# Kernel tuning notes

Hardware: AMD Instinct MI355X
Metric: run time of the kernel (lower is better)

## Reference

```python
import jax, jax.numpy as jnp
import numpy as np

N_NODES = 100000
BN_EPS = 1e-5


def _linear_params(key, fan_in, fan_out):
    k1, k2 = jax.random.split(key)
    lim = 1.0 / np.sqrt(fan_in)
    W = jax.random.uniform(k1, (fan_in, fan_out), jnp.float32, -lim, lim)
    b = jax.random.uniform(k2, (fan_out,), jnp.float32, -lim, lim)
    return W, b


def setup_inputs() -> dict:
    key = jax.random.key(0)
    ks = jax.random.split(key, 24)
    in_ch, hid, tdim, L = 17, 64, 32, 2
    E = 1600000
    inp = {}
    inp["x"] = jax.random.normal(ks[0], (N_NODES, in_ch), jnp.float32)
    inp["edge_index"] = jax.random.randint(ks[1], (2, E), 0, N_NODES, jnp.int64)
    inp["edge_dts"] = jax.random.uniform(ks[2], (E,), jnp.float32) * 100.0
    inp["batch_size"] = 10000
    # TimeEncode params (learned, TGAT init)
    inp["basis_freq"] = jnp.asarray(1.0 / 10 ** np.linspace(0, 9, tdim), jnp.float32)
    inp["phase"] = jnp.zeros((tdim,), jnp.float32)
    # TMP edge MLP: in = 2*in_ch + tdim
    mi = 2 * in_ch + tdim
    inp["tmp_W1"], inp["tmp_b1"] = _linear_params(ks[3], mi, mi // 2)
    inp["tmp_W2"], inp["tmp_b2"] = _linear_params(ks[4], mi // 2, in_ch)
    inp["proj_W"], inp["proj_b"] = _linear_params(ks[5], in_ch, hid)
    # SMP layers (stacked over L)
    si = 2 * hid
    W1s, b1s, W2s, b2s = [], [], [], []
    for l in range(L):
        W1, b1 = _linear_params(ks[6 + 2 * l], si, si // 2)
        W2, b2 = _linear_params(ks[7 + 2 * l], si // 2, hid)
        W1s.append(W1); b1s.append(b1); W2s.append(W2); b2s.append(b2)
    inp["smp_W1"] = jnp.stack(W1s); inp["smp_b1"] = jnp.stack(b1s)
    inp["smp_W2"] = jnp.stack(W2s); inp["smp_b2"] = jnp.stack(b2s)
    inp["bn_gamma"] = jnp.ones((L, hid), jnp.float32)
    inp["bn_beta"] = jnp.zeros((L, hid), jnp.float32)
    # classifier head
    inp["clf_W1"], inp["clf_b1"] = _linear_params(ks[12], hid, hid)
    inp["clf_g1"] = jnp.ones((hid,), jnp.float32); inp["clf_bb1"] = jnp.zeros((hid,), jnp.float32)
    inp["clf_W2"], inp["clf_b2"] = _linear_params(ks[13], hid, hid // 2)
    inp["clf_g2"] = jnp.ones((hid // 2,), jnp.float32); inp["clf_bb2"] = jnp.zeros((hid // 2,), jnp.float32)
    inp["clf_W3"], inp["clf_b3"] = _linear_params(ks[14], hid // 2, 1)
    return inp


def _segment_mean(vals, idx, n):
    s = jax.ops.segment_sum(vals, idx, num_segments=n)
    c = jax.ops.segment_sum(jnp.ones((idx.shape[0], 1), vals.dtype), idx, num_segments=n)
    return s / jnp.maximum(c, 1.0)


def _bn(x, g, b):
    m = x.mean(0)
    v = x.var(0)
    return (x - m) * jax.lax.rsqrt(v + BN_EPS) * g + b


def reference(x, edge_index, edge_dts, batch_size, basis_freq, phase,
              tmp_W1, tmp_b1, tmp_W2, tmp_b2, proj_W, proj_b,
              smp_W1, smp_b1, smp_W2, smp_b2, bn_gamma, bn_beta,
              clf_W1, clf_b1, clf_g1, clf_bb1,
              clf_W2, clf_b2, clf_g2, clf_bb2, clf_W3, clf_b3):
    src, dst = edge_index[0], edge_index[1]  # x_j = x[src], x_i = x[dst]
    n = x.shape[0]
    # TimeEncode: cos(t * freq + phase)  -> [E, time_dim]
    rel = jnp.cos(edge_dts[:, None] * basis_freq + phase)
    # --- TMP conv (applied once) ---
    x_i = x[dst]
    m_in = jnp.concatenate([x_i, x[src], rel], axis=-1)
    p = jnp.tanh(jax.nn.relu(m_in @ tmp_W1 + tmp_b1) @ tmp_W2 + tmp_b2)
    msg = (2.0 * p - 1.0) * x_i  # (p - q) * x_i with q = 1 - p
    h = x + _segment_mean(msg, dst, n)
    # --- project to hidden ---
    h = h @ proj_W + proj_b
    # --- L SMP layers with BatchNorm + ReLU (dropout = eval/identity) ---
    L = smp_W1.shape[0]
    for l in range(L):
        h_i = h[dst]
        m_in = jnp.concatenate([h_i, h[src]], axis=-1)
        p = jnp.tanh(jax.nn.relu(m_in @ smp_W1[l] + smp_b1[l]) @ smp_W2[l] + smp_b2[l])
        h = h + _segment_mean((2.0 * p - 1.0) * h_i, dst, n)
        h = jax.nn.relu(_bn(h, bn_gamma[l], bn_beta[l]))
    # --- classifier on seed nodes ---
    z = h[:batch_size]
    z = jax.nn.relu(_bn(z @ clf_W1 + clf_b1, clf_g1, clf_bb1))
    z = jax.nn.relu(_bn(z @ clf_W2 + clf_b2, clf_g2, clf_bb2))
    return z @ clf_W3 + clf_b3  # [batch_size, 1] logits
```

## Files before the change

### kernel.cpp

```cpp
#include <hip/hip_runtime.h>
#include <hip/hip_bf16.h>


typedef float  f32x4 __attribute__((ext_vector_type(4)));
typedef short  s16x8 __attribute__((ext_vector_type(8)));

__device__ __forceinline__ float tanh_factor(float u) {
  float e = __expf(2.0f * u);
  return fmaf(-4.0f, __builtin_amdgcn_rcpf(e + 1.0f), 1.0f);
}

__device__ __forceinline__ void atomic_add_f32(float* p, float v) {
  unsafeAtomicAdd(p, v);
}

__device__ __forceinline__ unsigned short f2bf(float f) {
  __hip_bfloat16 b = __float2bfloat16(f);
  return *(unsigned short*)&b;
}
__device__ __forceinline__ float bf2f(unsigned short u) {
  unsigned int v = ((unsigned int)u) << 16;
  return *(float*)&v;
}

__global__ __launch_bounds__(256) void k_hist(
    const int* __restrict__ ei, int* __restrict__ cntI, int E)
{
  int e = blockIdx.x * 256 + threadIdx.x;
  if (e < E) atomicAdd(&cntI[ei[E + e]], 1);
}

__global__ __launch_bounds__(256) void k_scan_block(
    const int* __restrict__ cntI, int* __restrict__ cursor,
    int* __restrict__ bsum, int N)
{
  __shared__ int s[256];
  const int t = threadIdx.x;
  int i = blockIdx.x * 256 + t;
  int v = (i < N) ? cntI[i] : 0;
  s[t] = v;
  for (int off = 1; off < 256; off <<= 1) {
    __syncthreads();
    int x = (t >= off) ? s[t - off] : 0;
    __syncthreads();
    s[t] += x;
  }
  __syncthreads();
  if (i < N) cursor[i] = s[t] - v;
  if (t == 255) bsum[blockIdx.x] = s[255];
}

__global__ __launch_bounds__(512) void k_scan_bsum(int* __restrict__ bsum, int nb)
{
  __shared__ int s[512];
  const int t = threadIdx.x;
  int v = (t < nb) ? bsum[t] : 0;
  s[t] = v;
  for (int off = 1; off < 512; off <<= 1) {
    __syncthreads();
    int x = (t >= off) ? s[t - off] : 0;
    __syncthreads();
    s[t] += x;
  }
  __syncthreads();
  if (t < nb) bsum[t] = s[t] - v;
}

__global__ __launch_bounds__(256) void k_expand_add(
    int* __restrict__ cursor, const int* __restrict__ bsum,
    const int* __restrict__ cntI, int* __restrict__ dstS, int N)
{
  int n = blockIdx.x * 256 + threadIdx.x;
  if (n >= N) return;
  int cur = cursor[n] + bsum[blockIdx.x];
  cursor[n] = cur;
  int c = cntI[n];
  for (int i = 0; i < c; i++) dstS[cur + i] = n;
}

__global__ __launch_bounds__(256) void k_scatter(
    const int* __restrict__ ei, const float* __restrict__ dts,
    int* __restrict__ cursor, int2* __restrict__ srcdtS, int E)
{
  int e = blockIdx.x * 256 + threadIdx.x;
  if (e >= E) return;
  int d = ei[E + e];
  int pos = atomicAdd(&cursor[d], 1);
  srcdtS[pos] = make_int2(ei[e], __float_as_int(dts[e]));
}

__global__ __launch_bounds__(256) void prep_all(
    const float* __restrict__ x, const float* __restrict__ tW1,
    const float* __restrict__ tW2, const float* __restrict__ sW1,
    const float* __restrict__ sW2, unsigned short* __restrict__ xb,
    unsigned short* __restrict__ W1t1, unsigned short* __restrict__ W2t1,
    unsigned short* __restrict__ W1t, unsigned short* __restrict__ W2t, int N)
{
  int i = blockIdx.x * 256 + threadIdx.x;
  int totalX = N * 24;
  for (int idx = i; idx < totalX; idx += gridDim.x * 256) {
    int n = idx / 24, c = idx - n * 24;
    xb[idx] = (c < 17) ? f2bf(x[n * 17 + c]) : (unsigned short)0;
  }
  if (i < 48 * 96) {
    int n = i / 96, k = i - n * 96;
    int src = (k < 17) ? k : (k >= 24 && k < 41) ? (k - 24 + 17)
            : (k >= 48 && k < 80) ? (k - 48 + 34) : -1;
    W1t1[i] = (n < 33 && src >= 0) ? f2bf(tW1[src * 33 + n]) : (unsigned short)0;
  }
  if (i < 32 * 64) {
    int n = i / 64, k = i - n * 64;
    W2t1[i] = (n < 17 && k < 33) ? f2bf(tW2[k * 17 + n]) : (unsigned short)0;
  }
  if (i < 2 * 64 * 128) {
    int l = i >> 13; int r = i & 8191; int n = r >> 7; int k = r & 127;
    W1t[i] = f2bf(sW1[((size_t)l * 128 + k) * 64 + n]);
  }
  if (i < 2 * 64 * 64) {
    int l = i >> 12; int r = i & 4095; int n = r >> 6; int k = r & 63;
    W2t[i] = f2bf(sW2[((size_t)l * 64 + k) * 64 + n]);
  }
}

__global__ __launch_bounds__(256, 3) void phase1_edge_mfma(
    const unsigned short* __restrict__ xb, const int* __restrict__ dstS,
    const int2* __restrict__ srcdtS, const float* __restrict__ freq,
    const float* __restrict__ phs,
    const unsigned short* __restrict__ W1t1, const float* __restrict__ b1,
    const unsigned short* __restrict__ W2t1, const float* __restrict__ b2,
    float* __restrict__ accum, int E, int nwt)
{
  __shared__ unsigned short sA[64][104];
  __shared__ unsigned short sHid[64][72];
  __shared__ float sRed[64][20];
  __shared__ int   sDst[64];

  const int t = threadIdx.x;
  const int wv = t >> 6, lane = t & 63, l16 = lane & 15, quad = lane >> 4;
  const int r0 = wv * 16;

  s16x8 w1f[3][3], w2f[2][2];
  float bias1[3], bias2[2];
#pragma unroll
  for (int cb = 0; cb < 3; cb++) {
    int n = cb * 16 + l16;
#pragma unroll
    for (int kb = 0; kb < 3; kb++)
      w1f[cb][kb] = *(const s16x8*)&W1t1[n * 96 + kb * 32 + quad * 8];
    bias1[cb] = (n < 33) ? b1[n] : 0.0f;
  }
#pragma unroll
  for (int cb = 0; cb < 2; cb++) {
    int n = cb * 16 + l16;
#pragma unroll
    for (int kb = 0; kb < 2; kb++)
      w2f[cb][kb] = *(const s16x8*)&W2t1[n * 64 + kb * 32 + quad * 8];
    bias2[cb] = (n < 17) ? b2[n] : 0.0f;
  }

  for (int i = lane; i < 16 * 28; i += 64) {
    int rr = r0 + i / 28, c = i % 28;
    int col = (c < 6) ? 18 + c : (c < 12) ? 42 + (c - 6) : 80 + (c - 12);
    sA[rr][col] = 0;
  }
  for (int i = lane; i < 256; i += 64)
    sHid[r0 + (i >> 4)][48 + (i & 15)] = 0;

  const int gw = blockIdx.x * 4 + wv;
  const int nw = gridDim.x * 4;

  for (int tile = gw; tile < nwt; tile += nw) {
    const int eb = tile << 4;

    {
      int e_loc = lane >> 2, q = lane & 3;
      int rr = r0 + e_loc;
      int er = eb + e_loc; if (er >= E) er = E - 1;
      if (q < 2) {
        int node = q ? srcdtS[er].x : dstS[er];
        if (!q) sDst[rr] = node;
        const unsigned short* src = &xb[(size_t)node * 24];
        int base = q ? 24 : 0;
        *(uint4*)&sA[rr][base]     = *(const uint4*)&src[0];
        *(uint4*)&sA[rr][base + 8] = *(const uint4*)&src[8];
        *(unsigned int*)&sA[rr][base + 16] = *(const unsigned int*)&src[16];
      } else {
        float dt = __int_as_float(srcdtS[er].y);
        int k0 = (q == 2) ? 0 : 16;
        unsigned short tmp[16] __attribute__((aligned(16)));
#pragma unroll
        for (int j = 0; j < 16; j++)
          tmp[j] = f2bf(__cosf(fmaf(dt, freq[k0 + j], phs[k0 + j])));
        *(uint4*)&sA[rr][48 + k0]     = *(const uint4*)&tmp[0];
        *(uint4*)&sA[rr][48 + k0 + 8] = *(const uint4*)&tmp[8];
      }
    }

    f32x4 a1[3];
#pragma unroll
    for (int cb = 0; cb < 3; cb++)
      a1[cb] = (f32x4){bias1[cb], bias1[cb], bias1[cb], bias1[cb]};
#pragma unroll
    for (int kb = 0; kb < 3; kb++) {
      s16x8 aF = *(const s16x8*)&sA[r0 + l16][kb * 32 + quad * 8];
#pragma unroll
      for (int cb = 0; cb < 3; cb++)
        a1[cb] = __builtin_amdgcn_mfma_f32_16x16x32_bf16(aF, w1f[cb][kb], a1[cb], 0, 0, 0);
    }
#pragma unroll
    for (int cb = 0; cb < 3; cb++)
#pragma unroll
      for (int reg = 0; reg < 4; reg++)
        sHid[r0 + quad * 4 + reg][cb * 16 + l16] = f2bf(fmaxf(a1[cb][reg], 0.0f));

    f32x4 a2[2];
#pragma unroll
    for (int cb = 0; cb < 2; cb++)
      a2[cb] = (f32x4){bias2[cb], bias2[cb], bias2[cb], bias2[cb]};
#pragma unroll
    for (int kb = 0; kb < 2; kb++) {
      s16x8 aF = *(const s16x8*)&sHid[r0 + l16][kb * 32 + quad * 8];
#pragma unroll
      for (int cb = 0; cb < 2; cb++)
        a2[cb] = __builtin_amdgcn_mfma_f32_16x16x32_bf16(aF, w2f[cb][kb], a2[cb], 0, 0, 0);
    }

#pragma unroll
    for (int reg = 0; reg < 4; reg++) {
      int row = r0 + quad * 4 + reg;
      bool ok = (eb + quad * 4 + reg < E);
      sRed[row][l16] = ok ? tanh_factor(a2[0][reg]) : 0.0f;
      if (l16 == 0) sRed[row][16] = ok ? tanh_factor(a2[1][reg]) : 0.0f;
    }

    if (lane < 17) {
      int col = lane;
      float run = 0.0f;
      int cur = sDst[r0];
#pragma unroll
      for (int k = 0; k < 16; k++) {
        int d = sDst[r0 + k];
        float v = sRed[r0 + k][col];
        if (d != cur) {
          atomic_add_f32(&accum[(size_t)cur * 17 + col], run);
          run = 0.0f; cur = d;
        }
        run += v;
      }
      atomic_add_f32(&accum[(size_t)cur * 17 + col], run);
    }
  }
}

__global__ __launch_bounds__(256) void phase1_node(
    const float* __restrict__ x, const float* __restrict__ acc1,
    const int* __restrict__ cntI, const float* __restrict__ Wp,
    const float* __restrict__ bp, float* __restrict__ h, int N)
{
  __shared__ float s0[4][20];
  const int t = threadIdx.x;
  const int nb = blockIdx.x << 2;
  if (t < 68) {
    int nl = t / 17, c = t % 17;
    int n = nb + nl;
    float v = 0.0f;
    if (n < N) {
      float cnt = fmaxf((float)cntI[n], 1.0f);
      v = x[n * 17 + c] * (1.0f + acc1[n * 17 + c] / cnt);
    }
    s0[nl][c] = v;
  }
  __syncthreads();
  int nl = t >> 6, j = t & 63;
  int n = nb + nl;
  if (n < N) {
    float acc = bp[j];
#pragma unroll
    for (int c = 0; c < 17; c++) acc = fmaf(s0[nl][c], Wp[c * 64 + j], acc);
    h[n * 64 + j] = acc;
  }
}

__global__ void prep_P(
    const float* __restrict__ h, const unsigned short* __restrict__ W1t,
    const float* __restrict__ b1, unsigned short* __restrict__ P1,
    unsigned short* __restrict__ P2, int N)
{
  __shared__ unsigned short sH[64][72];
  const int t = threadIdx.x;
  const int wv = t >> 6, lane = t & 63, l16 = lane & 15, quad = lane >> 4;
  const int nb = blockIdx.x << 6;

#pragma unroll
  for (int i = 0; i < 4; i++) {
    int g = t + i * 256;
    int r = g >> 4, c4 = (g & 15) << 2;
    int n = nb + r; if (n >= N) n = N - 1;
    float4 v = *(const float4*)&h[(size_t)n * 64 + c4];
    ushort4 o = { f2bf(v.x), f2bf(v.y), f2bf(v.z), f2bf(v.w) };
    *(ushort4*)&sH[r][c4] = o;
  }
  __syncthreads();

  const int n = nb + wv * 16 + l16;
#pragma unroll
  for (int half = 0; half < 2; half++) {
    f32x4 acc[4];
#pragma unroll
    for (int cb = 0; cb < 4; cb++) {
      if (half == 0) {
        float4 bv = *(const float4*)&b1[cb * 16 + quad * 4];
        acc[cb] = (f32x4){bv.x, bv.y, bv.z, bv.w};
      } else {
        acc[cb] = (f32x4){0.0f, 0.0f, 0.0f, 0.0f};
      }
    }
#pragma unroll
    for (int kb = 0; kb < 2; kb++) {
      s16x8 bF = *(const s16x8*)&sH[wv * 16 + l16][kb * 32 + quad * 8];
#pragma unroll
      for (int cb = 0; cb < 4; cb++) {
        s16x8 aF = *(const s16x8*)&W1t[(cb * 16 + l16) * 128 + half * 64 + kb * 32 + quad * 8];
        acc[cb] = __builtin_amdgcn_mfma_f32_16x16x32_bf16(aF, bF, acc[cb], 0, 0, 0);
      }
    }
    if (n < N) {
      unsigned short* P = half ? P2 : P1;
#pragma unroll
      for (int cb = 0; cb < 4; cb++) {
        ushort4 o = { f2bf(acc[cb][0]), f2bf(acc[cb][1]),
                      f2bf(acc[cb][2]), f2bf(acc[cb][3]) };
        *(ushort4*)&P[(size_t)n * 64 + cb * 16 + quad * 4] = o;
      }
    }
  }
}

__global__ __launch_bounds__(256, 4) void phase2_edge(
    const unsigned short* __restrict__ P1, const unsigned short* __restrict__ P2,
    const int* __restrict__ dstS, const int2* __restrict__ srcdtS,
    const unsigned short* __restrict__ W2t, const float* __restrict__ b2,
    float* __restrict__ accum, int E, int nwt)
{
  __shared__ unsigned short sA[64][136];
  __shared__ int sDst[64];
  float* sRedF = (float*)&sA[0][0];

  const int t = threadIdx.x;
  const int wv = t >> 6, lane = t & 63, l16 = lane & 15, quad = lane >> 4;
  const int r0 = wv * 16;

  s16x8 w2f[4][2];
  f32x4 bias2v[4];
#pragma unroll
  for (int cb = 0; cb < 4; cb++) {
#pragma unroll
    for (int kb = 0; kb < 2; kb++)
      w2f[cb][kb] = *(const s16x8*)&W2t[(cb * 16 + l16) * 64 + kb * 32 + quad * 8];
    float4 bv = *(const float4*)&b2[cb * 16 + quad * 4];
    bias2v[cb] = (f32x4){bv.x, bv.y, bv.z, bv.w};
  }

  const int gw = blockIdx.x * 4 + wv;
  const int nw = gridDim.x * 4;
  const int eRow = r0 + l16;

  for (int tile = gw; tile < nwt; tile += nw) {
    const int eb = tile << 4;

    {
      int e_loc = lane >> 2, q = lane & 3;
      int rr = r0 + e_loc;
      int er = eb + e_loc; if (er >= E) er = E - 1;
      int node;
      if (q < 2) { node = dstS[er]; if (!q) sDst[rr] = node; }
      else       node = srcdtS[er].x;
      const unsigned short* src = (q < 2 ? P1 : P2) + (size_t)node * 64 + (q & 1) * 32;
      int cb0 = q * 32;
#pragma unroll
      for (int j = 0; j < 4; j++)
        *(uint4*)&sA[rr][cb0 + j * 8] = *(const uint4*)&src[j * 8];
    }

    s16x8 hidf[2];
#pragma unroll
    for (int kb = 0; kb < 2; kb++) {
      s16x8 x1 = *(const s16x8*)&sA[eRow][kb * 32 + quad * 8];
      s16x8 x2 = *(const s16x8*)&sA[eRow][64 + kb * 32 + quad * 8];
      s16x8 hf;
#pragma unroll
      for (int j = 0; j < 8; j++) {
        float a = bf2f((unsigned short)x1[j]);
        float b = bf2f((unsigned short)x2[j]);
        hf[j] = (short)f2bf(fmaxf(a + b, 0.0f));
      }
      hidf[kb] = hf;
    }

    f32x4 acc[4];
#pragma unroll
    for (int cb = 0; cb < 4; cb++) acc[cb] = bias2v[cb];
#pragma unroll
    for (int kb = 0; kb < 2; kb++)
#pragma unroll
      for (int cb = 0; cb < 4; cb++)
        acc[cb] = __builtin_amdgcn_mfma_f32_16x16x32_bf16(w2f[cb][kb], hidf[kb], acc[cb], 0, 0, 0);

    bool ok = (eb + l16 < E);
#pragma unroll
    for (int cb = 0; cb < 4; cb++) {
      f32x4 f;
#pragma unroll
      for (int reg = 0; reg < 4; reg++)
        f[reg] = ok ? tanh_factor(acc[cb][reg]) : 0.0f;
      *(f32x4*)&sRedF[eRow * 68 + cb * 16 + quad * 4] = f;
    }

    {
      float run = 0.0f;
      int cur = sDst[r0];
#pragma unroll
      for (int k = 0; k < 16; k++) {
        int d = sDst[r0 + k];
        float v = sRedF[(r0 + k) * 68 + lane];
        if (d != cur) {
          atomic_add_f32(&accum[(size_t)cur * 64 + lane], run);
          run = 0.0f; cur = d;
        }
        run += v;
      }
      atomic_add_f32(&accum[(size_t)cur * 64 + lane], run);
    }
  }
}

__global__ __launch_bounds__(256) void node_update_bn(
    float* __restrict__ h, float* __restrict__ accum,
    const int* __restrict__ cntI, float* __restrict__ bns,
    float* __restrict__ bnq, int N)
{
  const int t = threadIdx.x;
  float ls = 0.0f, lq = 0.0f;
  int total = N * 64;
  for (int idx = blockIdx.x * 256 + t; idx < total; idx += gridDim.x * 256) {
    int n = idx >> 6;
    float cnt = fmaxf((float)cntI[n], 1.0f);
    float v = h[idx] * (1.0f + accum[idx] / cnt);
    accum[idx] = 0.0f;
    h[idx] = v;
    ls += v; lq += v * v;
  }
  __shared__ float ss[256], sq[256];
  ss[t] = ls; sq[t] = lq;
  __syncthreads();
  if (t < 64) {
    float s = ss[t] + ss[t + 64] + ss[t + 128] + ss[t + 192];
    float q = sq[t] + sq[t + 64] + sq[t + 128] + sq[t + 192];
    atomic_add_f32(&bns[t], s);
    atomic_add_f32(&bnq[t], q);
  }
}

__global__ __launch_bounds__(256) void bn_apply_relu(
    float* __restrict__ d, const float* __restrict__ bns,
    const float* __restrict__ bnq, const float* __restrict__ gam,
    const float* __restrict__ bet, int total, int cmask, float invRows)
{
  for (int idx = blockIdx.x * 256 + threadIdx.x; idx < total;
       idx += gridDim.x * 256) {
    int c = idx & cmask;
    float m = bns[c] * invRows;
    float var = bnq[c] * invRows - m * m;
    float sc = gam[c] * rsqrtf(var + 1e-5f);
    d[idx] = fmaxf((d[idx] - m) * sc + bet[c], 0.0f);
  }
}

__global__ __launch_bounds__(256) void clf_mm_bn(
    const float* __restrict__ in, const float* __restrict__ W,
    const float* __restrict__ b, float* __restrict__ out,
    float* __restrict__ bns, float* __restrict__ bnq,
    int rows, int K, int cshift)
{
  const int t = threadIdx.x;
  const int C = 1 << cshift;
  int total = rows << cshift;
  float ls = 0.0f, lq = 0.0f;
  for (int idx = blockIdx.x * 256 + t; idx < total; idx += gridDim.x * 256) {
    int n = idx >> cshift;
    int c = idx & (C - 1);
    float acc = b[c];
#pragma unroll 8
    for (int k = 0; k < K; k++) acc = fmaf(in[n * K + k], W[(k << cshift) + c], acc);
    out[idx] = acc;
    ls += acc; lq += acc * acc;
  }
  __shared__ float ss[256], sq[256];
  ss[t] = ls; sq[t] = lq;
  __syncthreads();
  if (t < C) {
    float s = 0.0f, q = 0.0f;
    for (int i = t; i < 256; i += C) { s += ss[i]; q += sq[i]; }
    atomic_add_f32(&bns[t], s);
    atomic_add_f32(&bnq[t], q);
  }
}

__global__ __launch_bounds__(256) void clf_final(
    const float* __restrict__ z2, const float* __restrict__ W3,
    const float* __restrict__ b3, float* __restrict__ out, int rows)
{
  int n = blockIdx.x * 256 + threadIdx.x;
  if (n >= rows) return;
  float acc = b3[0];
#pragma unroll
  for (int k = 0; k < 32; k++) acc = fmaf(z2[n * 32 + k], W3[k], acc);
  out[n] = acc;
}

extern "C" void kernel_launch(void* const* d_in, const int* in_sizes, int n_in,
                              void* d_out, int out_size, void* d_ws, size_t ws_size,
                              hipStream_t stream)
{
  const float* x    = (const float*)d_in[0];
  const int*   ei   = (const int*)  d_in[1];
  const float* dts  = (const float*)d_in[2];
  const float* freq = (const float*)d_in[4];
  const float* phs  = (const float*)d_in[5];
  const float* tW1  = (const float*)d_in[6];
  const float* tb1  = (const float*)d_in[7];
  const float* tW2  = (const float*)d_in[8];
  const float* tb2  = (const float*)d_in[9];
  const float* pW   = (const float*)d_in[10];
  const float* pb   = (const float*)d_in[11];
  const float* sW1  = (const float*)d_in[12];
  const float* sb1  = (const float*)d_in[13];
  const float* sW2  = (const float*)d_in[14];
  const float* sb2  = (const float*)d_in[15];
  const float* bng  = (const float*)d_in[16];
  const float* bnb  = (const float*)d_in[17];
  const float* cW1  = (const float*)d_in[18];
  const float* cb1  = (const float*)d_in[19];
  const float* cg1  = (const float*)d_in[20];
  const float* cbb1 = (const float*)d_in[21];
  const float* cW2  = (const float*)d_in[22];
  const float* cb2  = (const float*)d_in[23];
  const float* cg2  = (const float*)d_in[24];
  const float* cbb2 = (const float*)d_in[25];
  const float* cW3  = (const float*)d_in[26];
  const float* cb3  = (const float*)d_in[27];
  float* out = (float*)d_out;

  const int N = in_sizes[0] / 17;
  const int E = in_sizes[1] / 2;
  const int B = out_size;

  char* base = (char*)d_ws;
  size_t off = 0;
  float* h    = (float*)(base + off); off += (size_t)N * 64 * 4;
  float* acc2 = (float*)(base + off); off += (size_t)N * 64 * 4;
  char*  uni  = base + off;           off += (size_t)N * 64 * 4;
  float* bnsAll = (float*)(base + off); off += 8 * 64 * 4;
  unsigned short* W1t = (unsigned short*)(base + off); off += 2 * 64 * 128 * 2;
  unsigned short* W2t = (unsigned short*)(base + off); off += 2 * 64 * 64 * 2;
  int* cntI   = (int*)(base + off); off += (size_t)N * 4;
  int* cursor = (int*)(base + off); off += (size_t)N * 4;
  int* bsum   = (int*)(base + off); off += 512 * 4;
  int* dstS   = (int*)(base + off); off += (size_t)E * 4;
  off = (off + 15) & ~(size_t)15;
  int2* srcdtS = (int2*)(base + off); off += (size_t)E * 8;
  size_t needed = off;
  if (ws_size < needed) return;

  float* acc1 = (float*)uni;
  unsigned short* xb   = (unsigned short*)(uni + (size_t)N * 17 * 4);
  unsigned short* W1t1 = xb + (size_t)N * 24;
  unsigned short* W2t1 = W1t1 + 48 * 96;
  unsigned short* P1 = (unsigned short*)uni;
  unsigned short* P2 = P1 + (size_t)N * 64;
  float* z1 = (float*)uni;
  float* z2 = z1 + (size_t)B * 64;

  const int nwt = (E + 15) / 16;
  const int NB = (N + 255) / 256;
  if (NB > 512) return;

  hipMemsetAsync(cntI, 0, (size_t)N * 4, stream);
  hipMemsetAsync(acc1, 0, (size_t)N * 17 * 4, stream);
  hipMemsetAsync(acc2, 0, (size_t)N * 64 * 4, stream);
  hipMemsetAsync(bnsAll, 0, 8 * 64 * 4, stream);

  k_hist<<<(E + 255) / 256, 256, 0, stream>>>(ei, cntI, E);
  k_scan_block<<<NB, 256, 0, stream>>>(cntI, cursor, bsum, N);
  k_scan_bsum<<<1, 512, 0, stream>>>(bsum, NB);
  k_expand_add<<<NB, 256, 0, stream>>>(cursor, bsum, cntI, dstS, N);
  k_scatter<<<(E + 255) / 256, 256, 0, stream>>>(ei, dts, cursor, srcdtS, E);
  prep_all<<<(N * 24 + 255) / 256, 256, 0, stream>>>(
      x, tW1, tW2, sW1, sW2, xb, W1t1, W2t1, W1t, W2t, N);

  phase1_edge_mfma<<<768, 256, 0, stream>>>(
      xb, dstS, srcdtS, freq, phs, W1t1, tb1, W2t1, tb2, acc1, E, nwt);
  phase1_node<<<(N + 3) / 4, 256, 0, stream>>>(x, acc1, cntI, pW, pb, h, N);

  for (int l = 0; l < 2; l++) {
    float* bns = bnsAll + l * 128;
    float* bnq = bns + 64;
    prep_P<<<(N + 63) / 64, 256, 0, stream>>>(
        h, W1t + (size_t)l * 64 * 128, sb1 + l * 64, P1, P2, N);
    phase2_edge<<<1024, 256, 0, stream>>>(
        P1, P2, dstS, srcdtS, W2t + (size_t)l * 64 * 64, sb2 + l * 64,
        acc2, E, nwt);
    node_update_bn<<<1024, 256, 0, stream>>>(h, acc2, cntI, bns, bnq, N);
    bn_apply_relu<<<2048, 256, 0, stream>>>(
        h, bns, bnq, bng + l * 64, bnb + l * 64, N * 64, 63, 1.0f / (float)N);
  }

  {
    float* bns = bnsAll + 256;
    float* bnq = bns + 64;
    clf_mm_bn<<<2500, 256, 0, stream>>>(h, cW1, cb1, z1, bns, bnq, B, 64, 6);
    bn_apply_relu<<<1024, 256, 0, stream>>>(z1, bns, bnq, cg1, cbb1,
                                            B * 64, 63, 1.0f / (float)B);
  }
  {
    float* bns = bnsAll + 384;
    float* bnq = bns + 64;
    clf_mm_bn<<<1250, 256, 0, stream>>>(z1, cW2, cb2, z2, bns, bnq, B, 64, 5);
    bn_apply_relu<<<512, 256, 0, stream>>>(z2, bns, bnq, cg2, cbb2,
                                           B * 32, 31, 1.0f / (float)B);
  }
  clf_final<<<(B + 255) / 256, 256, 0, stream>>>(z2, cW3, cb3, out, B);
}
```

Before: 876.2 us.

## Use bf16 MFMA for classifier matmuls and nontemporal loads for edge streams

Replaces the scalar FMA classifier matmul-plus-BN-stats kernel with a templated MFMA kernel. It stages 64 input rows in LDS as bf16 and reduces the BN statistics with warp shuffles. The classifier weights are pre-transposed to bf16 in prep_all. Separately, edge-index, dt and sorted-edge stream reads in several kernels now use nontemporal loads to reduce cache pollution. The bf16 conversion lowers precision in the classifier head.

```diff
diff --git a/kernel.cpp b/kernel.cpp
--- a/kernel.cpp
+++ b/kernel.cpp
@@ -27,7 +27,7 @@
     const int* __restrict__ ei, int* __restrict__ cntI, int E)
 {
   int e = blockIdx.x * 256 + threadIdx.x;
-  if (e < E) atomicAdd(&cntI[ei[E + e]], 1);
+  if (e < E) atomicAdd(&cntI[__builtin_nontemporal_load(ei + E + e)], 1);
 }
 
 __global__ __launch_bounds__(256) void k_scan_block(
@@ -84,17 +84,21 @@
 {
   int e = blockIdx.x * 256 + threadIdx.x;
   if (e >= E) return;
-  int d = ei[E + e];
+  int d = __builtin_nontemporal_load(ei + E + e);
+  int s = __builtin_nontemporal_load(ei + e);
+  float dt = __builtin_nontemporal_load(dts + e);
   int pos = atomicAdd(&cursor[d], 1);
-  srcdtS[pos] = make_int2(ei[e], __float_as_int(dts[e]));
+  srcdtS[pos] = make_int2(s, __float_as_int(dt));
 }
 
 __global__ __launch_bounds__(256) void prep_all(
     const float* __restrict__ x, const float* __restrict__ tW1,
     const float* __restrict__ tW2, const float* __restrict__ sW1,
-    const float* __restrict__ sW2, unsigned short* __restrict__ xb,
+    const float* __restrict__ sW2, const float* __restrict__ cW1,
+    const float* __restrict__ cW2, unsigned short* __restrict__ xb,
     unsigned short* __restrict__ W1t1, unsigned short* __restrict__ W2t1,
-    unsigned short* __restrict__ W1t, unsigned short* __restrict__ W2t, int N)
+    unsigned short* __restrict__ W1t, unsigned short* __restrict__ W2t,
+    unsigned short* __restrict__ cW1t, unsigned short* __restrict__ cW2t, int N)
 {
   int i = blockIdx.x * 256 + threadIdx.x;
   int totalX = N * 24;
@@ -119,6 +123,14 @@
   if (i < 2 * 64 * 64) {
     int l = i >> 12; int r = i & 4095; int n = r >> 6; int k = r & 63;
     W2t[i] = f2bf(sW2[((size_t)l * 64 + k) * 64 + n]);
+  }
+  if (i < 64 * 64) {
+    int c = i >> 6, k = i & 63;
+    cW1t[i] = f2bf(cW1[k * 64 + c]);
+  }
+  if (i < 32 * 64) {
+    int c = i >> 6, k = i & 63;
+    cW2t[i] = f2bf(cW2[k * 32 + c]);
   }
 }
 
@@ -177,7 +189,8 @@
       int rr = r0 + e_loc;
       int er = eb + e_loc; if (er >= E) er = E - 1;
       if (q < 2) {
-        int node = q ? srcdtS[er].x : dstS[er];
+        int node = q ? __builtin_nontemporal_load(&srcdtS[er].x)
+                     : __builtin_nontemporal_load(dstS + er);
         if (!q) sDst[rr] = node;
         const unsigned short* src = &xb[(size_t)node * 24];
         int base = q ? 24 : 0;
@@ -185,7 +198,7 @@
         *(uint4*)&sA[rr][base + 8] = *(const uint4*)&src[8];
         *(unsigned int*)&sA[rr][base + 16] = *(const unsigned int*)&src[16];
       } else {
-        float dt = __int_as_float(srcdtS[er].y);
+        float dt = __int_as_float(__builtin_nontemporal_load(&srcdtS[er].y));
         int k0 = (q == 2) ? 0 : 16;
         unsigned short tmp[16] __attribute__((aligned(16)));
 #pragma unroll
@@ -373,8 +386,12 @@
       int rr = r0 + e_loc;
       int er = eb + e_loc; if (er >= E) er = E - 1;
       int node;
-      if (q < 2) { node = dstS[er]; if (!q) sDst[rr] = node; }
-      else       node = srcdtS[er].x;
+      if (q < 2) {
+        node = __builtin_nontemporal_load(dstS + er);
+        if (!q) sDst[rr] = node;
+      } else {
+        node = __builtin_nontemporal_load(&srcdtS[er].x);
+      }
       const unsigned short* src = (q < 2 ? P1 : P2) + (size_t)node * 64 + (q & 1) * 32;
       int cb0 = q * 32;
 #pragma unroll
@@ -476,33 +493,79 @@
   }
 }
 
-__global__ __launch_bounds__(256) void clf_mm_bn(
-    const float* __restrict__ in, const float* __restrict__ W,
-    const float* __restrict__ b, float* __restrict__ out,
-    float* __restrict__ bns, float* __restrict__ bnq,
-    int rows, int K, int cshift)
-{
-  const int t = threadIdx.x;
-  const int C = 1 << cshift;
-  int total = rows << cshift;
-  float ls = 0.0f, lq = 0.0f;
-  for (int idx = blockIdx.x * 256 + t; idx < total; idx += gridDim.x * 256) {
-    int n = idx >> cshift;
-    int c = idx & (C - 1);
-    float acc = b[c];
-#pragma unroll 8
-    for (int k = 0; k < K; k++) acc = fmaf(in[n * K + k], W[(k << cshift) + c], acc);
-    out[idx] = acc;
-    ls += acc; lq += acc * acc;
-  }
-  __shared__ float ss[256], sq[256];
-  ss[t] = ls; sq[t] = lq;
+template <int NCB>
+__global__ __launch_bounds__(256) void clf_mfma(
+    const float* __restrict__ in, const unsigned short* __restrict__ Wt,
+    const float* __restrict__ bias, float* __restrict__ z,
+    float* __restrict__ bns, float* __restrict__ bnq, int rows)
+{
+  __shared__ unsigned short sIn[64][72];
+  const int t = threadIdx.x;
+  const int wv = t >> 6, lane = t & 63, l16 = lane & 15, quad = lane >> 4;
+  const int nb = blockIdx.x << 6;
+
+  s16x8 wf[NCB][2];
+  f32x4 bv[NCB];
+#pragma unroll
+  for (int cb = 0; cb < NCB; cb++) {
+#pragma unroll
+    for (int kb = 0; kb < 2; kb++)
+      wf[cb][kb] = *(const s16x8*)&Wt[(cb * 16 + l16) * 64 + kb * 32 + quad * 8];
+    float4 b4 = *(const float4*)&bias[cb * 16 + quad * 4];
+    bv[cb] = (f32x4){b4.x, b4.y, b4.z, b4.w};
+  }
+
+#pragma unroll
+  for (int i = 0; i < 4; i++) {
+    int g = t + i * 256;
+    int r = g >> 4, c4 = (g & 15) << 2;
+    int n = nb + r; if (n >= rows) n = rows - 1;
+    float4 v = *(const float4*)&in[(size_t)n * 64 + c4];
+    ushort4 o = { f2bf(v.x), f2bf(v.y), f2bf(v.z), f2bf(v.w) };
+    *(ushort4*)&sIn[r][c4] = o;
+  }
   __syncthreads();
-  if (t < C) {
-    float s = 0.0f, q = 0.0f;
-    for (int i = t; i < 256; i += C) { s += ss[i]; q += sq[i]; }
-    atomic_add_f32(&bns[t], s);
-    atomic_add_f32(&bnq[t], q);
+
+  const int n = nb + wv * 16 + l16;
+  const bool ok = (n < rows);
+  f32x4 acc[NCB];
+#pragma unroll
+  for (int cb = 0; cb < NCB; cb++) acc[cb] = bv[cb];
+#pragma unroll
+  for (int kb = 0; kb < 2; kb++) {
+    s16x8 bF = *(const s16x8*)&sIn[wv * 16 + l16][kb * 32 + quad * 8];
+#pragma unroll
+    for (int cb = 0; cb < NCB; cb++)
+      acc[cb] = __builtin_amdgcn_mfma_f32_16x16x32_bf16(wf[cb][kb], bF, acc[cb], 0, 0, 0);
+  }
+
+#pragma unroll
+  for (int cb = 0; cb < NCB; cb++) {
+    if (ok)
+      *(float4*)&z[(size_t)n * (NCB * 16) + cb * 16 + quad * 4] =
+          make_float4(acc[cb][0], acc[cb][1], acc[cb][2], acc[cb][3]);
+    f32x4 s, q;
+#pragma unroll
+    for (int reg = 0; reg < 4; reg++) {
+      float v = ok ? acc[cb][reg] : 0.0f;
+      s[reg] = v; q[reg] = v * v;
+    }
+#pragma unroll
+    for (int m = 1; m < 16; m <<= 1) {
+#pragma unroll
+      for (int reg = 0; reg < 4; reg++) {
+        s[reg] += __shfl_xor(s[reg], m);
+        q[reg] += __shfl_xor(q[reg], m);
+      }
+    }
+    if (l16 == 0) {
+#pragma unroll
+      for (int reg = 0; reg < 4; reg++) {
+        int col = cb * 16 + quad * 4 + reg;
+        atomic_add_f32(&bns[col], s[reg]);
+        atomic_add_f32(&bnq[col], q[reg]);
+      }
+    }
   }
 }
 
@@ -563,6 +626,8 @@
   float* bnsAll = (float*)(base + off); off += 8 * 64 * 4;
   unsigned short* W1t = (unsigned short*)(base + off); off += 2 * 64 * 128 * 2;
   unsigned short* W2t = (unsigned short*)(base + off); off += 2 * 64 * 64 * 2;
+  unsigned short* cW1t = (unsigned short*)(base + off); off += 64 * 64 * 2;
+  unsigned short* cW2t = (unsigned short*)(base + off); off += 32 * 64 * 2;
   int* cntI   = (int*)(base + off); off += (size_t)N * 4;
   int* cursor = (int*)(base + off); off += (size_t)N * 4;
   int* bsum   = (int*)(base + off); off += 512 * 4;
@@ -596,7 +661,7 @@
   k_expand_add<<<NB, 256, 0, stream>>>(cursor, bsum, cntI, dstS, N);
   k_scatter<<<(E + 255) / 256, 256, 0, stream>>>(ei, dts, cursor, srcdtS, E);
   prep_all<<<(N * 24 + 255) / 256, 256, 0, stream>>>(
-      x, tW1, tW2, sW1, sW2, xb, W1t1, W2t1, W1t, W2t, N);
+      x, tW1, tW2, sW1, sW2, cW1, cW2, xb, W1t1, W2t1, W1t, W2t, cW1t, cW2t, N);
 
   phase1_edge_mfma<<<768, 256, 0, stream>>>(
       xb, dstS, srcdtS, freq, phs, W1t1, tb1, W2t1, tb2, acc1, E, nwt);
@@ -615,17 +680,18 @@
         h, bns, bnq, bng + l * 64, bnb + l * 64, N * 64, 63, 1.0f / (float)N);
   }
 
+  const int CB = (B + 63) / 64;
   {
     float* bns = bnsAll + 256;
     float* bnq = bns + 64;
-    clf_mm_bn<<<2500, 256, 0, stream>>>(h, cW1, cb1, z1, bns, bnq, B, 64, 6);
+    clf_mfma<4><<<CB, 256, 0, stream>>>(h, cW1t, cb1, z1, bns, bnq, B);
     bn_apply_relu<<<1024, 256, 0, stream>>>(z1, bns, bnq, cg1, cbb1,
                                             B * 64, 63, 1.0f / (float)B);
   }
   {
     float* bns = bnsAll + 384;
     float* bnq = bns + 64;
-    clf_mm_bn<<<1250, 256, 0, stream>>>(z1, cW2, cb2, z2, bns, bnq, B, 64, 5);
+    clf_mfma<2><<<CB, 256, 0, stream>>>(z1, cW2t, cb2, z2, bns, bnq, B);
     bn_apply_relu<<<512, 256, 0, stream>>>(z2, bns, bnq, cg2, cbb2,
                                            B * 32, 31, 1.0f / (float)B);
   }
```

New measurement: 935.8 us. 6.8% more time.
